# Kernel optimization log

Measured on AMD Instinct MI355X. Metric: run time of the kernel, lower is better.

Reference implementation:

```python
import jax, jax.numpy as jnp
import numpy as np

N_NODES = 1024

def gcn_conv(x, src, dst, W, b):
    # x: [B, N, Fin]; symmetric-normalized GCN with self loops (PyG GCNConv)
    B, N, _ = x.shape
    loops = jnp.arange(N, dtype=src.dtype)
    s = jnp.concatenate([src, loops])
    d = jnp.concatenate([dst, loops])
    deg = jnp.zeros((N,), x.dtype).at[d].add(1.0)
    dis = jax.lax.rsqrt(deg)                      # deg >= 1 due to self loops
    norm = dis[s] * dis[d]                        # [E+N]
    xw = x @ W                                    # [B, N, Fout]
    msgs = xw[:, s, :] * norm[None, :, None]      # gather along node dim
    out = jnp.zeros_like(xw).at[:, d, :].add(msgs)
    return out + b

def setup_inputs() -> dict:
    key = jax.random.key(0)
    ks = jax.random.split(key, 12)
    B, T, N, F = 8, 16, N_NODES, 8
    E = 32 * N
    n_in, n_hid, n_out = T * F, 256, 128
    def xavier(k, fan_in, fan_out):
        std = np.sqrt(2.0 / (fan_in + fan_out))
        return jax.random.normal(k, (fan_in, fan_out), jnp.float32) * std
    return {
        "x": jax.random.normal(ks[0], (B, T, N, F), jnp.float32),
        "edge_index": jax.random.randint(ks[1], (2, E), 0, N, jnp.int64 if jax.config.jax_enable_x64 else jnp.int32),
        "m_in": jax.random.uniform(ks[2], (E, N), jnp.float32),
        "m_out": jax.random.uniform(ks[3], (E, N), jnp.float32),
        "W1": xavier(ks[4], n_in, n_hid),
        "b1": jnp.full((n_hid,), 0.1, jnp.float32),
        "Wm": xavier(ks[5], 2 * n_hid, n_hid),
        "bm": jnp.full((n_hid,), 0.1, jnp.float32),
        "W2": xavier(ks[6], n_hid, n_out),
        "b2": jnp.full((n_out,), 0.1, jnp.float32),
    }

def reference(x, edge_index, m_in, m_out, W1, b1, Wm, bm, W2, b2):
    B = x.shape[0]
    N = x.shape[2]
    x = x.reshape(B, N, -1)                          # x.view(B, N, -1)
    src, dst = edge_index[0], edge_index[1]
    h = jax.nn.relu(gcn_conv(x, src, dst, W1, b1))   # conv1 + relu
    # node2edge (batched over samples instead of python loop)
    e = jnp.concatenate([
        jnp.einsum('en,bnf->bef', m_in, h),
        jnp.einsum('en,bnf->bef', m_out, h),
    ], axis=-1)                                      # [B, E, 2*n_hid]
    e = jax.nn.relu(e @ Wm + bm)                     # mlp1 + relu (dropout p=0 -> identity)
    # edge2node: incoming = m_in^T @ e, mean-normalized by node count
    h2 = jnp.einsum('en,bef->bnf', m_in, e) / N
    return gcn_conv(h2, src, dst, W2, b2)            # conv2
```

## Files before the change

kernel.cpp:

```cpp
#include <hip/hip_runtime.h>
#include <hip/hip_bf16.h>

typedef __attribute__((ext_vector_type(8))) short bf16x8;
typedef __attribute__((ext_vector_type(4))) float f32x4;

static constexpr int NB   = 8;
static constexpr int NN   = 1024;
static constexpr int NE   = 32768;
static constexpr int FIN  = 128;
static constexpr int FH   = 256;
static constexpr int FOUT = 128;
static constexpr int MR   = NB * NN;

__device__ __forceinline__ short f2bf(float f) {
  union { __hip_bfloat16 h; short s; } u;
  u.h = __float2bfloat16(f);
  return u.s;
}

typedef const __attribute__((address_space(1))) void gas_void;
typedef __attribute__((address_space(3))) void las_void;
__device__ __forceinline__ void glds16(short* lds, const short* g) {
  __builtin_amdgcn_global_load_lds((gas_void*)g, (las_void*)lds, 16, 0, 0);
}
__device__ __forceinline__ void BAR() {
  asm volatile("" ::: "memory");
  __builtin_amdgcn_s_barrier();
  asm volatile("" ::: "memory");
}

__global__ void k_deg(const int* __restrict__ dst, int* __restrict__ deg) {
  int e = blockIdx.x * blockDim.x + threadIdx.x;
  if (e < NE) atomicAdd(&deg[dst[e]], 1);
}
__global__ void k_dis(const int* __restrict__ deg, float* __restrict__ dis) {
  int n = blockIdx.x * blockDim.x + threadIdx.x;
  if (n < NN) dis[n] = rsqrtf((float)(deg[n] + 1));
}
__global__ void k_adj(const int* __restrict__ src, const int* __restrict__ dst,
                      const float* __restrict__ dis, float* __restrict__ Adj) {
  int t = blockIdx.x * blockDim.x + threadIdx.x;
  if (t < NE) {
    int s = src[t], d = dst[t];
    atomicAdd(&Adj[d * NN + s], dis[s] * dis[d]);
  } else if (t < NE + NN) {
    int n = t - NE;
    atomicAdd(&Adj[n * NN + n], dis[n] * dis[n]);
  }
}

__global__ __launch_bounds__(256) void k_cast(const float4* __restrict__ S,
                                              short* __restrict__ D) {
  size_t q = (size_t)blockIdx.x * 256 + threadIdx.x;
  float4 a = S[q];
  short4 p;
  p.x = f2bf(a.x); p.y = f2bf(a.y); p.z = f2bf(a.z); p.w = f2bf(a.w);
  *(short4*)&D[q * 4] = p;
}
__global__ __launch_bounds__(256) void k_wt(const float* __restrict__ W1,
                                            const float* __restrict__ Wm,
                                            const float* __restrict__ W2,
                                            short* __restrict__ W1T,
                                            short* __restrict__ WmT,
                                            short* __restrict__ W2T) {
  int idx = blockIdx.x * 256 + threadIdx.x;
  if (idx < 128 * 256) {
    int r = idx >> 8, c = idx & 255;
    W1T[c * 128 + r] = f2bf(W1[idx]);
  } else if (idx < 128 * 256 + 512 * 256) {
    int k = idx - 128 * 256;
    int r = k >> 8, c = k & 255;
    int h = r >> 8, kk = r & 255;
    WmT[h * 65536 + c * 256 + kk] = f2bf(Wm[k]);
  } else {
    int k = idx - 128 * 256 - 512 * 256;
    int r = k >> 7, c = k & 127;
    W2T[c * 256 + r] = f2bf(W2[k]);
  }
}
__global__ __launch_bounds__(256) void k_prep(const float* __restrict__ mi,
                                              const float* __restrict__ mo,
                                              short* __restrict__ mi_bf,
                                              short* __restrict__ mo_bf,
                                              short* __restrict__ miT) {
  __shared__ short tile[64][72];
  int tid = threadIdx.x;
  int e0 = blockIdx.x * 64, n0 = blockIdx.y * 64;
  if (blockIdx.z == 1) {
    #pragma unroll
    for (int i = 0; i < 16; ++i) {
      int r = i * 4 + (tid >> 6), c = tid & 63;
      mo_bf[(size_t)(e0 + r) * 1024 + n0 + c] =
          f2bf(mo[(size_t)(e0 + r) * 1024 + n0 + c]);
    }
    return;
  }
  #pragma unroll
  for (int i = 0; i < 16; ++i) {
    int r = i * 4 + (tid >> 6), c = tid & 63;
    short v = f2bf(mi[(size_t)(e0 + r) * 1024 + n0 + c]);
    tile[c][r] = v;
    mi_bf[(size_t)(e0 + r) * 1024 + n0 + c] = v;
  }
  __syncthreads();
  int n = tid >> 2, ec = (tid & 3) * 16;
  #pragma unroll
  for (int q = 0; q < 4; ++q) {
    short4 v;
    v.x = tile[n][ec + q * 4 + 0];
    v.y = tile[n][ec + q * 4 + 1];
    v.z = tile[n][ec + q * 4 + 2];
    v.w = tile[n][ec + q * 4 + 3];
    *(short4*)&miT[(size_t)(n0 + n) * 32768 + e0 + ec + q * 4] = v;
  }
}
__global__ __launch_bounds__(256) void k_repack2(const float* __restrict__ H2X,
                                                 short* __restrict__ XW2T) {
  __shared__ float t[32][33];
  int n0 = blockIdx.x * 32, c0 = blockIdx.y * 32;
  int r = threadIdx.x >> 5, cc = threadIdx.x & 31;
  #pragma unroll
  for (int p = 0; p < 4; ++p)
    t[r + p * 8][cc] = H2X[(size_t)(n0 + r + p * 8) * 1024 + c0 + cc];
  __syncthreads();
  const float inv = 1.0f / 1024.0f;
  #pragma unroll
  for (int p = 0; p < 4; ++p) {
    int c = c0 + r + p * 8;
    int b = c >> 7, f = c & 127;
    XW2T[(size_t)f * 8192 + b * 1024 + n0 + cc] = f2bf(t[cc][r + p * 8] * inv);
  }
}

template <int EPI, int ASRC, int BSEL, bool BIAS, bool RELU>
__launch_bounds__(256)
__global__ void gemm_mfma(const short* __restrict__ Ab, const float* __restrict__ Af,
                          const short* __restrict__ BT, const float* __restrict__ bias,
                          void* __restrict__ Cv,
                          int lda, int ldb, int ldc, int K, int kSplit, int nz2,
                          int zcolB, size_t szA, size_t szB, size_t szC, size_t szC2,
                          float scale) {
  __shared__ __align__(16) short As[128 * 64];
  __shared__ __align__(16) short Bs[128 * 64];

  const int tid = threadIdx.x;
  const int lane = tid & 63, wid = tid >> 6;
  const int wr = wid >> 1, wc = wid & 1;
  const int fr = lane & 15, fq = lane >> 4;
  const int m0 = blockIdx.y * 128, n0 = blockIdx.x * 128;

  int zA = 0, zB = 0, k0 = 0, k1 = K;
  if constexpr (EPI == 1) {
    k0 = blockIdx.z * kSplit; k1 = k0 + kSplit;
  } else {
    zA = (int)blockIdx.z % nz2; zB = (int)blockIdx.z / nz2;
  }
  if constexpr (ASRC == 0) Ab += (size_t)zA * szA;
  else                     Af += (size_t)zA * szA;
  BT += (size_t)zB * szB;
  const int colB = zB * zcolB;

  const int rq = lane >> 3;
  const int ks = (lane & 7) ^ rq;

  f32x4 acc[4][4] = {};

  for (int kt = k0; kt < k1; kt += 64) {
    if constexpr (ASRC == 2) {
      #pragma unroll
      for (int p = 0; p < 4; ++p) {
        int i = p * 256 + tid, row = i >> 3, g = i & 7;
        const float* ap = Af + (size_t)(m0 + row) * lda + kt + g * 8;
        bf16x8 v;
        #pragma unroll
        for (int e = 0; e < 8; ++e) v[e] = f2bf(ap[e]);
        *(bf16x8*)&As[row * 64 + ((g ^ (row & 7)) * 8)] = v;
      }
    } else {
      #pragma unroll
      for (int c = 0; c < 4; ++c) {
        int row = wid * 32 + c * 8 + rq;
        glds16(&As[(wid * 256 + c * 64) * 8],
               Ab + (size_t)(m0 + row) * lda + kt + ks * 8);
      }
    }
    {
      const short* Bsrc;
      int ldbe;
      if constexpr (BSEL == 1) { Bsrc = BT + colB; ldbe = 8192; }
      else                     { Bsrc = BT;        ldbe = ldb;  }
      #pragma unroll
      for (int c = 0; c < 4; ++c) {
        int row = wid * 32 + c * 8 + rq;
        glds16(&Bs[(wid * 256 + c * 64) * 8],
               Bsrc + (size_t)(n0 + row) * ldbe + kt + ks * 8);
      }
    }
    __syncthreads();
    bf16x8 afv[4][2], bfv[4][2];
    #pragma unroll
    for (int i = 0; i < 4; ++i) {
      int row = wr * 64 + i * 16 + fr;
      #pragma unroll
      for (int kh = 0; kh < 2; ++kh)
        afv[i][kh] = *(const bf16x8*)&As[row * 64 + (((kh * 4 + fq) ^ (fr & 7)) * 8)];
    }
    #pragma unroll
    for (int j = 0; j < 4; ++j) {
      int row = wc * 64 + j * 16 + fr;
      #pragma unroll
      for (int kh = 0; kh < 2; ++kh)
        bfv[j][kh] = *(const bf16x8*)&Bs[row * 64 + (((kh * 4 + fq) ^ (fr & 7)) * 8)];
    }
    #pragma unroll
    for (int i = 0; i < 4; ++i)
      #pragma unroll
      for (int j = 0; j < 4; ++j) {
        acc[i][j] = __builtin_amdgcn_mfma_f32_16x16x32_bf16(afv[i][0], bfv[j][0], acc[i][j], 0, 0, 0);
        acc[i][j] = __builtin_amdgcn_mfma_f32_16x16x32_bf16(afv[i][1], bfv[j][1], acc[i][j], 0, 0, 0);
      }
    __syncthreads();
  }

  const size_t cOff = (size_t)zB * szC + (size_t)zA * szC2;
  #pragma unroll
  for (int i = 0; i < 4; ++i) {
    int rowb = m0 + wr * 64 + i * 16 + fq * 4;
    #pragma unroll
    for (int j = 0; j < 4; ++j) {
      int col = n0 + wc * 64 + j * 16 + fr;
      float bv = 0.0f;
      if constexpr (BIAS) bv = bias[col];
      float v0 = acc[i][j][0] + bv, v1 = acc[i][j][1] + bv;
      float v2 = acc[i][j][2] + bv, v3 = acc[i][j][3] + bv;
      if constexpr (RELU) {
        v0 = fmaxf(v0, 0.0f); v1 = fmaxf(v1, 0.0f);
        v2 = fmaxf(v2, 0.0f); v3 = fmaxf(v3, 0.0f);
      }
      if constexpr (EPI == 0) {
        short* Ct = (short*)Cv + cOff;
        short4 pk;
        pk.x = f2bf(v0); pk.y = f2bf(v1); pk.z = f2bf(v2); pk.w = f2bf(v3);
        *(short4*)(Ct + (size_t)col * ldc + rowb) = pk;
      } else if constexpr (EPI == 1) {
        float* Cf = (float*)Cv;
        atomicAdd(&Cf[(size_t)(rowb + 0) * ldc + col], acc[i][j][0] * scale);
        atomicAdd(&Cf[(size_t)(rowb + 1) * ldc + col], acc[i][j][1] * scale);
        atomicAdd(&Cf[(size_t)(rowb + 2) * ldc + col], acc[i][j][2] * scale);
        atomicAdd(&Cf[(size_t)(rowb + 3) * ldc + col], acc[i][j][3] * scale);
      } else if constexpr (EPI == 2) {
        short* Cn = (short*)Cv + cOff;
        Cn[(size_t)(rowb + 0) * ldc + col] = f2bf(v0);
        Cn[(size_t)(rowb + 1) * ldc + col] = f2bf(v1);
        Cn[(size_t)(rowb + 2) * ldc + col] = f2bf(v2);
        Cn[(size_t)(rowb + 3) * ldc + col] = f2bf(v3);
      } else {
        float* Cf = (float*)Cv + cOff;
        Cf[(size_t)(rowb + 0) * ldc + col] = v0;
        Cf[(size_t)(rowb + 1) * ldc + col] = v1;
        Cf[(size_t)(rowb + 2) * ldc + col] = v2;
        Cf[(size_t)(rowb + 3) * ldc + col] = v3;
      }
    }
  }
}

__launch_bounds__(512, 2)
__global__ void egemm8(const short* __restrict__ Ain, const short* __restrict__ Aout,
                       const short* __restrict__ G2T, const float* __restrict__ bm,
                       short* __restrict__ Ebn, int e0) {
  __shared__ __align__(16) short As[2][16384];
  __shared__ __align__(16) short Bs[2][16384];

  const int tid = threadIdx.x;
  const int lane = tid & 63, wid = tid >> 6;
  const int wm = wid >> 2, wn = wid & 3;
  const int fr = lane & 15, fq = lane >> 4;
  const int m0 = blockIdx.y * 256;
  const int n0 = blockIdx.x * 256;
  const size_t arow0 = (size_t)(e0 + m0) * 1024;

  const int rl = tid >> 3;
  const int ce = ((tid & 7) ^ (rl & 7)) << 3;
  const int ldst = wid << 9;

  f32x4 acc[8][4] = {};

  auto stageA = [&](int buf, int kt, int iss) {
    const short* s = (kt < 1024 ? Ain : Aout) + arow0
                   + (size_t)(iss * 64 + rl) * 1024 + (kt & 1023) + ce;
    glds16(&As[buf][iss * 4096 + ldst], s);
  };
  auto stageB = [&](int buf, int kt, int iss) {
    const short* s = G2T + (size_t)(n0 + iss * 64 + rl) * 2048 + kt + ce;
    glds16(&Bs[buf][iss * 4096 + ldst], s);
  };

#define EG_PHASE(QM, QN, STAGES, WAITOP)                                          \
  {                                                                               \
    bf16x8 af[4][2], bv[2][2];                                                    \
    _Pragma("unroll")                                                             \
    for (int i = 0; i < 4; ++i) {                                                 \
      int r = wm * 128 + ((QM) * 4 + i) * 16 + fr;                                \
      _Pragma("unroll")                                                           \
      for (int s = 0; s < 2; ++s)                                                 \
        af[i][s] = *(const bf16x8*)&As[buf][r * 64 + (((s * 4 + fq) ^ (r & 7)) << 3)]; \
    }                                                                             \
    _Pragma("unroll")                                                             \
    for (int j = 0; j < 2; ++j) {                                                 \
      int rb = wn * 64 + ((QN) * 2 + j) * 16 + fr;                                \
      _Pragma("unroll")                                                           \
      for (int s = 0; s < 2; ++s)                                                 \
        bv[j][s] = *(const bf16x8*)&Bs[buf][rb * 64 + (((s * 4 + fq) ^ (rb & 7)) << 3)]; \
    }                                                                             \
    STAGES                                                                        \
    WAITOP                                                                        \
    BAR();                                                                        \
    asm volatile("s_waitcnt lgkmcnt(0)" ::: "memory");                            \
    __builtin_amdgcn_s_setprio(1);                                                \
    _Pragma("unroll")                                                             \
    for (int i = 0; i < 4; ++i)                                                   \
      _Pragma("unroll")                                                           \
      for (int j = 0; j < 2; ++j) {                                               \
        acc[(QM) * 4 + i][(QN) * 2 + j] = __builtin_amdgcn_mfma_f32_16x16x32_bf16(\
            af[i][0], bv[j][0], acc[(QM) * 4 + i][(QN) * 2 + j], 0, 0, 0);        \
        acc[(QM) * 4 + i][(QN) * 2 + j] = __builtin_amdgcn_mfma_f32_16x16x32_bf16(\
            af[i][1], bv[j][1], acc[(QM) * 4 + i][(QN) * 2 + j], 0, 0, 0);        \
      }                                                                           \
    __builtin_amdgcn_s_setprio(0);                                                \
    BAR();                                                                        \
  }

  #pragma unroll
  for (int i = 0; i < 4; ++i) stageA(0, 0, i);
  #pragma unroll
  for (int i = 0; i < 4; ++i) stageB(0, 0, i);
  asm volatile("s_waitcnt vmcnt(0)" ::: "memory");
  BAR();

  constexpr int NT = 2048 / 64;
  for (int t = 0; t < NT; ++t) {
    const int buf = t & 1, nb = buf ^ 1, ktn = (t + 1) * 64;
    const bool pre = (t + 1 < NT);
    EG_PHASE(0, 0, { if (pre) { stageA(nb, ktn, 0); stageA(nb, ktn, 2); } }, ;)
    EG_PHASE(0, 1, { if (pre) { stageB(nb, ktn, 0); stageB(nb, ktn, 1); } },
             asm volatile("s_waitcnt vmcnt(4)" ::: "memory");)
    EG_PHASE(1, 0, { if (pre) { stageB(nb, ktn, 2); stageB(nb, ktn, 3); } }, ;)
    EG_PHASE(1, 1, { if (pre) { stageA(nb, ktn, 1); stageA(nb, ktn, 3); } },
             asm volatile("s_waitcnt vmcnt(2)" ::: "memory");)
  }
#undef EG_PHASE

  #pragma unroll
  for (int i = 0; i < 8; ++i) {
    int e = m0 + wm * 128 + i * 16 + fq * 4;
    #pragma unroll
    for (int j = 0; j < 4; ++j) {
      int col = n0 + wn * 64 + j * 16 + fr;
      float bb = bm[col & 255];
      Ebn[(size_t)(e + 0) * 2048 + col] = f2bf(fmaxf(acc[i][j][0] + bb, 0.0f));
      Ebn[(size_t)(e + 1) * 2048 + col] = f2bf(fmaxf(acc[i][j][1] + bb, 0.0f));
      Ebn[(size_t)(e + 2) * 2048 + col] = f2bf(fmaxf(acc[i][j][2] + bb, 0.0f));
      Ebn[(size_t)(e + 3) * 2048 + col] = f2bf(fmaxf(acc[i][j][3] + bb, 0.0f));
    }
  }
}

extern "C" void kernel_launch(void* const* d_in, const int* in_sizes, int n_in,
                              void* d_out, int out_size, void* d_ws, size_t ws_size,
                              hipStream_t stream) {
  const float* x     = (const float*)d_in[0];
  const int*   ei    = (const int*)d_in[1];
  const float* m_in  = (const float*)d_in[2];
  const float* m_out = (const float*)d_in[3];
  const float* W1    = (const float*)d_in[4];
  const float* b1    = (const float*)d_in[5];
  const float* Wm    = (const float*)d_in[6];
  const float* bm    = (const float*)d_in[7];
  const float* W2    = (const float*)d_in[8];
  const float* b2    = (const float*)d_in[9];
  float* out = (float*)d_out;
  const int* src = ei;
  const int* dst = ei + NE;

  char* w = (char*)d_ws;
  size_t used = 0;
  auto alloc = [&](size_t bytes) {
    char* p = w; size_t r = (bytes + 255) & ~(size_t)255;
    w += r; used += r; return p;
  };
  float* dis    = (float*)alloc((size_t)NN * 4);
  int*   deg    = (int*)  alloc((size_t)NN * 4);
  short* Adjb   = (short*)alloc((size_t)NN * NN * 2);
  short* W1T    = (short*)alloc((size_t)FH * FIN * 2);
  short* WmT    = (short*)alloc((size_t)2 * FH * FH * 2);
  short* W2T    = (short*)alloc((size_t)FOUT * FH * 2);
  short* G2T    = (short*)alloc((size_t)2048 * 2048 * 2);
  float* H2X    = (float*)alloc((size_t)NN * 1024 * 4);
  short* m_in_bf  = (short*)alloc((size_t)NE * NN * 2);
  short* m_out_bf = (short*)alloc((size_t)NE * NN * 2);
  short* m_inT    = (short*)alloc((size_t)NN * NE * 2);

  int EC = 4096;
  for (int ec : {32768, 16384, 8192}) {
    size_t need = (size_t)ec * 6144;
    if (need < (12u << 20)) need = 12u << 20;
    if (used + need + (1u << 20) <= ws_size) { EC = ec; break; }
  }
  size_t ubytes = (size_t)EC * 6144;
  if (ubytes < (12u << 20)) ubytes = 12u << 20;
  char* U = alloc(ubytes);
  float* Adj  = (float*)U;
  short* XW1T = (short*)(U + (4u << 20));
  short* Hb   = (short*)(U + (8u << 20));
  short* Ebn  = (short*)U;
  short* Dt   = (short*)(U + (size_t)EC * 4096);
  short* XW2T = (short*)U;

  const int nchunk = NE / EC;
  const int nsplit = (EC >= 16384) ? 16 : 8;

  hipMemsetAsync(deg, 0, (size_t)NN * 4, stream);
  hipMemsetAsync(Adj, 0, (size_t)NN * NN * 4, stream);
  hipMemsetAsync(H2X, 0, (size_t)NN * 1024 * 4, stream);

  k_deg<<<(NE + 255) / 256, 256, 0, stream>>>(dst, deg);
  k_dis<<<(NN + 255) / 256, 256, 0, stream>>>(deg, dis);
  k_adj<<<(NE + NN + 255) / 256, 256, 0, stream>>>(src, dst, dis, Adj);
  k_cast<<<NN * NN / 4 / 256, 256, 0, stream>>>((const float4*)Adj, Adjb);

  k_wt<<<(128 * 256 + 512 * 256 + 256 * 128) / 256, 256, 0, stream>>>(
      W1, Wm, W2, W1T, WmT, W2T);
  k_prep<<<dim3(NE / 64, NN / 64, 2), 256, 0, stream>>>(
      m_in, m_out, m_in_bf, m_out_bf, m_inT);

  gemm_mfma<0, 2, 0, false, false><<<dim3(2, 64, 1), 256, 0, stream>>>(
      nullptr, x, W1T, nullptr, XW1T, FIN, FIN, MR, FIN, 0, 1, 0, 0, 0, 0, 0, 1.0f);

  gemm_mfma<2, 0, 1, true, true><<<dim3(2, 8, NB), 256, 0, stream>>>(
      Adjb, nullptr, XW1T, b1, Hb,
      NN, 0, FH, NN, 0, 1, 1024, 0, 0, (size_t)NN * FH, 0, 1.0f);

  gemm_mfma<2, 0, 0, false, false><<<dim3(8, 2, 16), 256, 0, stream>>>(
      WmT, nullptr, Hb, nullptr, G2T,
      FH, FH, 2048, FH, 0, 2, 0,
      (size_t)FH * FH, (size_t)NN * FH, (size_t)FH * 2048, 1024, 1.0f);

  for (int c = 0; c < nchunk; ++c) {
    egemm8<<<dim3(8, EC / 256, 1), 512, 0, stream>>>(
        m_in_bf, m_out_bf, G2T, bm, Ebn, c * EC);
    gemm_mfma<2, 0, 0, false, false><<<dim3(EC / 128, 1, 8), 256, 0, stream>>>(
        W2T, nullptr, Ebn, nullptr, Dt,
        FH, 2048, EC, FH, 0, 1, 0,
        0, (size_t)FH, (size_t)FOUT * EC, 0, 1.0f);
    gemm_mfma<1, 0, 0, false, false><<<dim3(8, 8, nsplit), 256, 0, stream>>>(
        m_inT + (size_t)c * EC, nullptr, Dt, nullptr, H2X,
        32768, EC, 1024, EC, EC / nsplit, 1, 0, 0, 0, 0, 0, 1.0f);
  }

  k_repack2<<<dim3(32, 32), 256, 0, stream>>>(H2X, XW2T);

  gemm_mfma<3, 0, 1, true, false><<<dim3(1, 8, NB), 256, 0, stream>>>(
      Adjb, nullptr, XW2T, b2, out,
      NN, 0, FOUT, NN, 0, 1, 1024, 0, 0, (size_t)NN * FOUT, 0, 1.0f);
}
```

Measured before the change: 678.2 us.

## Fuse W2 projection into edge MLP GEMM epilogue via LDS staging

The edge-MLP GEMM epilogue now writes the bias+ReLU tile into shared memory instead of writing the bf16 edge activations to global memory. It then multiplies that tile by W2T with MFMA, loading the W2 fragments directly from global, and writes the projected Dt slice. This removes the separate W2 GEMM launch and the global round-trip of the large Ebn buffer, and the smaller workspace lets a larger edge chunk fit. The cost is extra register pressure for the W2 fragments and the second accumulator set, plus an additional barrier in the tail of a kernel that is already heavily tuned.

```diff
diff --git a/kernel.cpp b/kernel.cpp
--- a/kernel.cpp
+++ b/kernel.cpp
@@ -268,9 +268,11 @@
 __launch_bounds__(512, 2)
 __global__ void egemm8(const short* __restrict__ Ain, const short* __restrict__ Aout,
                        const short* __restrict__ G2T, const float* __restrict__ bm,
-                       short* __restrict__ Ebn, int e0) {
-  __shared__ __align__(16) short As[2][16384];
-  __shared__ __align__(16) short Bs[2][16384];
+                       const short* __restrict__ W2T, short* __restrict__ Dt,
+                       int e0, int EC) {
+  __shared__ __align__(16) short SMEM[65536];
+  short* As0 = SMEM;
+  short* Bs0 = SMEM + 32768;
 
   const int tid = threadIdx.x;
   const int lane = tid & 63, wid = tid >> 6;
@@ -289,11 +291,11 @@
   auto stageA = [&](int buf, int kt, int iss) {
     const short* s = (kt < 1024 ? Ain : Aout) + arow0
                    + (size_t)(iss * 64 + rl) * 1024 + (kt & 1023) + ce;
-    glds16(&As[buf][iss * 4096 + ldst], s);
+    glds16(&As0[buf * 16384 + iss * 4096 + ldst], s);
   };
   auto stageB = [&](int buf, int kt, int iss) {
     const short* s = G2T + (size_t)(n0 + iss * 64 + rl) * 2048 + kt + ce;
-    glds16(&Bs[buf][iss * 4096 + ldst], s);
+    glds16(&Bs0[buf * 16384 + iss * 4096 + ldst], s);
   };
 
 #define EG_PHASE(QM, QN, STAGES, WAITOP)                                          \
@@ -304,14 +306,14 @@
       int r = wm * 128 + ((QM) * 4 + i) * 16 + fr;                                \
       _Pragma("unroll")                                                           \
       for (int s = 0; s < 2; ++s)                                                 \
-        af[i][s] = *(const bf16x8*)&As[buf][r * 64 + (((s * 4 + fq) ^ (r & 7)) << 3)]; \
+        af[i][s] = *(const bf16x8*)&As0[buf * 16384 + r * 64 + (((s * 4 + fq) ^ (r & 7)) << 3)]; \
     }                                                                             \
     _Pragma("unroll")                                                             \
     for (int j = 0; j < 2; ++j) {                                                 \
       int rb = wn * 64 + ((QN) * 2 + j) * 16 + fr;                                \
       _Pragma("unroll")                                                           \
       for (int s = 0; s < 2; ++s)                                                 \
-        bv[j][s] = *(const bf16x8*)&Bs[buf][rb * 64 + (((s * 4 + fq) ^ (rb & 7)) << 3)]; \
+        bv[j][s] = *(const bf16x8*)&Bs0[buf * 16384 + rb * 64 + (((s * 4 + fq) ^ (rb & 7)) << 3)]; \
     }                                                                             \
     STAGES                                                                        \
     WAITOP                                                                        \
@@ -353,15 +355,53 @@
 
   #pragma unroll
   for (int i = 0; i < 8; ++i) {
-    int e = m0 + wm * 128 + i * 16 + fq * 4;
+    int eb = wm * 128 + i * 16 + fq * 4;
     #pragma unroll
     for (int j = 0; j < 4; ++j) {
-      int col = n0 + wn * 64 + j * 16 + fr;
-      float bb = bm[col & 255];
-      Ebn[(size_t)(e + 0) * 2048 + col] = f2bf(fmaxf(acc[i][j][0] + bb, 0.0f));
-      Ebn[(size_t)(e + 1) * 2048 + col] = f2bf(fmaxf(acc[i][j][1] + bb, 0.0f));
-      Ebn[(size_t)(e + 2) * 2048 + col] = f2bf(fmaxf(acc[i][j][2] + bb, 0.0f));
-      Ebn[(size_t)(e + 3) * 2048 + col] = f2bf(fmaxf(acc[i][j][3] + bb, 0.0f));
+      int f = wn * 64 + j * 16 + fr;
+      float bb = bm[f];
+      #pragma unroll
+      for (int r = 0; r < 4; ++r) {
+        int er = eb + r;
+        SMEM[er * 256 + ((((f >> 3) ^ (er & 7)) << 3) | (f & 7))] =
+            f2bf(fmaxf(acc[i][j][r] + bb, 0.0f));
+      }
+    }
+  }
+  asm volatile("s_waitcnt lgkmcnt(0)" ::: "memory");
+  BAR();
+  bf16x8 w2f[2][8];
+  #pragma unroll
+  for (int jj = 0; jj < 2; ++jj) {
+    int row = wn * 32 + jj * 16 + fr;
+    #pragma unroll
+    for (int kk = 0; kk < 8; ++kk)
+      w2f[jj][kk] = *(const bf16x8*)(W2T + (size_t)row * 256 + kk * 32 + fq * 8);
+  }
+  f32x4 dacc[8][2] = {};
+  #pragma unroll
+  for (int kk = 0; kk < 8; ++kk) {
+    #pragma unroll
+    for (int ii = 0; ii < 8; ++ii) {
+      int er = wm * 128 + ii * 16 + fr;
+      bf16x8 a = *(const bf16x8*)&SMEM[er * 256 + (((kk * 4 + fq) ^ (er & 7)) << 3)];
+      dacc[ii][0] = __builtin_amdgcn_mfma_f32_16x16x32_bf16(a, w2f[0][kk], dacc[ii][0], 0, 0, 0);
+      dacc[ii][1] = __builtin_amdgcn_mfma_f32_16x16x32_bf16(a, w2f[1][kk], dacc[ii][1], 0, 0, 0);
+    }
+  }
+  const int bx = blockIdx.x;
+  #pragma unroll
+  for (int ii = 0; ii < 8; ++ii) {
+    int e = m0 + wm * 128 + ii * 16 + fq * 4;
+    #pragma unroll
+    for (int jj = 0; jj < 2; ++jj) {
+      int frow = bx * 128 + wn * 32 + jj * 16 + fr;
+      short4 pk;
+      pk.x = f2bf(dacc[ii][jj][0]);
+      pk.y = f2bf(dacc[ii][jj][1]);
+      pk.z = f2bf(dacc[ii][jj][2]);
+      pk.w = f2bf(dacc[ii][jj][3]);
+      *(short4*)&Dt[(size_t)frow * EC + e] = pk;
     }
   }
 }
@@ -403,18 +443,17 @@
 
   int EC = 4096;
   for (int ec : {32768, 16384, 8192}) {
-    size_t need = (size_t)ec * 6144;
+    size_t need = (size_t)ec * 2048;
     if (need < (12u << 20)) need = 12u << 20;
     if (used + need + (1u << 20) <= ws_size) { EC = ec; break; }
   }
-  size_t ubytes = (size_t)EC * 6144;
+  size_t ubytes = (size_t)EC * 2048;
   if (ubytes < (12u << 20)) ubytes = 12u << 20;
   char* U = alloc(ubytes);
   float* Adj  = (float*)U;
   short* XW1T = (short*)(U + (4u << 20));
   short* Hb   = (short*)(U + (8u << 20));
-  short* Ebn  = (short*)U;
-  short* Dt   = (short*)(U + (size_t)EC * 4096);
+  short* Dt   = (short*)U;
   short* XW2T = (short*)U;
 
   const int nchunk = NE / EC;
@@ -448,11 +487,7 @@
 
   for (int c = 0; c < nchunk; ++c) {
     egemm8<<<dim3(8, EC / 256, 1), 512, 0, stream>>>(
-        m_in_bf, m_out_bf, G2T, bm, Ebn, c * EC);
-    gemm_mfma<2, 0, 0, false, false><<<dim3(EC / 128, 1, 8), 256, 0, stream>>>(
-        W2T, nullptr, Ebn, nullptr, Dt,
-        FH, 2048, EC, FH, 0, 1, 0,
-        0, (size_t)FH, (size_t)FOUT * EC, 0, 1.0f);
+        m_in_bf, m_out_bf, G2T, bm, W2T, Dt, c * EC, EC);
     gemm_mfma<1, 0, 0, false, false><<<dim3(8, 8, nsplit), 256, 0, stream>>>(
         m_inT + (size_t)c * EC, nullptr, Dt, nullptr, H2X,
         32768, EC, 1024, EC, EC / nsplit, 1, 0, 0, 0, 0, 0, 1.0f);
```

Result: faster. 614.8 us (-9.3%).
